# Optimization experiments

Hardware: AMD Instinct MI355X
Metric: run time of the kernel (lower is better)

Reference implementation:

```python
import jax, jax.numpy as jnp
import numpy as np

DIM = 512
NUM_HEADS = 8
HEAD_DIM = DIM // NUM_HEADS
SCALE = HEAD_DIM ** -0.5


def setup_inputs() -> dict:
    key = jax.random.key(0)
    k_x, k_qkv, k_proj, k_pb = jax.random.split(key, 4)
    x = jax.random.normal(k_x, (2, 4096, DIM), dtype=jnp.float32)
    # nn.Linear weights: stored as [out, in]; qkv_bias=False so no qkv bias.
    w_qkv = jax.random.normal(k_qkv, (3 * DIM, DIM), dtype=jnp.float32) * (DIM ** -0.5)
    w_proj = jax.random.normal(k_proj, (DIM, DIM), dtype=jnp.float32) * (DIM ** -0.5)
    b_proj = jax.random.normal(k_pb, (DIM,), dtype=jnp.float32) * 0.01
    return {"x": x, "w_qkv": w_qkv, "w_proj": w_proj, "b_proj": b_proj}


def reference(x, w_qkv, w_proj, b_proj):
    B, N, D = x.shape
    H, Hd = NUM_HEADS, HEAD_DIM
    # qkv: [B, N, 3D] -> [3, B, H, N, Hd]
    qkv = (x @ w_qkv.T).reshape(B, N, 3, H, Hd).transpose(2, 0, 3, 1, 4)
    q, k, v = qkv[0], qkv[1], qkv[2]
    # Naive full attention matrix in fp32 (matches original non-fused path).
    attn = jnp.einsum('bhqd,bhkd->bhqk', q, k) * SCALE
    attn = jax.nn.softmax(attn, axis=-1)
    out = jnp.einsum('bhqk,bhkd->bhqd', attn, v)
    out = out.transpose(0, 2, 1, 3).reshape(B, N, D)
    return out @ w_proj.T + b_proj
```

## Files before the change

### kernel.cpp

```cpp
#include <hip/hip_runtime.h>
#include <stdint.h>

#define SEQ   4096
#define DIMM  512
#define HDIM  64
#define NH    8
#define ROWS  8192
#define QKVN  1536

typedef __attribute__((ext_vector_type(8))) __bf16 bf16x8;
typedef __attribute__((ext_vector_type(4))) float  f32x4;
typedef __attribute__((ext_vector_type(4))) uint32_t u32x4;

__device__ __forceinline__ uint32_t cvtpk(float lo, float hi) {
  uint32_t w;
  asm("v_cvt_pk_bf16_f32 %0, %1, %2" : "=v"(w) : "v"(lo), "v"(hi));
  return w;
}

__device__ __forceinline__ void swap32(uint32_t& a, uint32_t& b) {
  asm("v_permlane32_swap_b32 %0, %1" : "+v"(a), "+v"(b));
}
__device__ __forceinline__ void swap16(uint32_t& a, uint32_t& b) {
  asm("v_permlane16_swap_b32 %0, %1" : "+v"(a), "+v"(b));
}

__device__ __forceinline__ f32x4 mfma16(bf16x8 a, bf16x8 b, f32x4 c) {
  return __builtin_amdgcn_mfma_f32_16x16x32_bf16(a, b, c, 0, 0, 0);
}

#if __has_builtin(__builtin_amdgcn_exp2f)
#define EXP2F(x) __builtin_amdgcn_exp2f(x)
#else
#define EXP2F(x) exp2f(x)
#endif

__device__ __forceinline__ void gld16(const void* g, void* l) {
  __builtin_amdgcn_global_load_lds(
      (const __attribute__((address_space(1))) uint32_t*)g,
      (__attribute__((address_space(3))) uint32_t*)l, 16, 0, 0);
}

#define X4  (ROWS * DIMM / 4)
#define Q4  (QKVN * DIMM / 4)
#define P4  (DIMM * DIMM / 4)

__global__ __launch_bounds__(256) void cvt_kernel(
    const float* __restrict__ x, const float* __restrict__ wq,
    const float* __restrict__ wp, uint16_t* __restrict__ xb,
    uint16_t* __restrict__ wqb, uint16_t* __restrict__ wpb) {
  int idx = blockIdx.x * 256 + threadIdx.x;
  const float* src; uint16_t* dst; int i4;
  if (idx < X4)            { src = x;  dst = xb;  i4 = idx; }
  else if (idx < X4 + Q4)  { src = wq; dst = wqb; i4 = idx - X4; }
  else                     { src = wp; dst = wpb; i4 = idx - X4 - Q4; }
  float4 v = ((const float4*)src)[i4];
  uint2 o;
  o.x = cvtpk(v.x, v.y);
  o.y = cvtpk(v.z, v.w);
  ((uint2*)dst)[i4] = o;
}

__device__ __forceinline__ void gemm_core(
    int bm, int bn,
    const uint16_t* __restrict__ A, const uint16_t* __restrict__ B,
    uint16_t (*As)[128 * 32], uint16_t (*Bs)[128 * 32], f32x4 acc[4][4]) {
  const int tid = threadIdx.x;
  const int lane = tid & 63, wave = tid >> 6;
  const int quad = lane >> 4, l16 = lane & 15;
  const int wr = (wave & 1) * 64, wc = (wave >> 1) * 64;
  const int sw = (l16 >> 1) & 3;

  auto stage = [&](int buf, int kt) {
#pragma unroll
    for (int it = 0; it < 2; ++it) {
      int L = it * 256 + tid;
      int r = L >> 2, c = L & 3;
      int gc = c ^ ((r >> 1) & 3);
      int ldsoff = (it * 256 + (tid & ~63)) * 16;
      gld16((const char*)A + ((size_t)(bm * 128 + r) * DIMM + kt * 32) * 2 + gc * 16,
            (char*)As[buf] + ldsoff);
      gld16((const char*)B + ((size_t)(bn * 128 + r) * DIMM + kt * 32) * 2 + gc * 16,
            (char*)Bs[buf] + ldsoff);
    }
  };

  stage(0, 0);
  for (int kt = 0; kt < DIMM / 32; ++kt) {
    const int cur = kt & 1;
    __syncthreads();
    if (kt < DIMM / 32 - 1) stage(cur ^ 1, kt + 1);

    bf16x8 af[4], bfr[4];
#pragma unroll
    for (int i = 0; i < 4; ++i)
      af[i] = *(const bf16x8*)(As[cur] + (wr + i * 16 + l16) * 32 + ((quad ^ sw) * 8));
#pragma unroll
    for (int j = 0; j < 4; ++j)
      bfr[j] = *(const bf16x8*)(Bs[cur] + (wc + j * 16 + l16) * 32 + ((quad ^ sw) * 8));
    __builtin_amdgcn_s_setprio(1);
#pragma unroll
    for (int i = 0; i < 4; ++i)
#pragma unroll
      for (int j = 0; j < 4; ++j)
        acc[i][j] = mfma16(af[i], bfr[j], acc[i][j]);
    __builtin_amdgcn_s_setprio(0);
  }
}

__global__ __launch_bounds__(256, 4) void qkv_gemm(
    const uint16_t* __restrict__ xb, const uint16_t* __restrict__ wqb,
    uint16_t* __restrict__ qd, uint16_t* __restrict__ kd,
    uint16_t* __restrict__ vt) {
  __shared__ __align__(16) uint16_t As[2][128 * 32];
  __shared__ __align__(16) uint16_t Bs[2][128 * 32];
  const int lin = blockIdx.y * 64 + blockIdx.x;
  const int bm = (lin & 7) * 8 + ((lin >> 3) / 12);
  const int bn = (lin >> 3) % 12;
  f32x4 acc[4][4];
#pragma unroll
  for (int i = 0; i < 4; ++i)
#pragma unroll
    for (int j = 0; j < 4; ++j) acc[i][j] = f32x4{0.f, 0.f, 0.f, 0.f};

  gemm_core(bm, bn, xb, wqb, As, Bs, acc);

  const int lane = threadIdx.x & 63, wave = threadIdx.x >> 6;
  const int quad = lane >> 4, l16 = lane & 15;
  const int wr = (wave & 1) * 64, wc = (wave >> 1) * 64;
  const float qscale = 0.125f * 1.44269504f;
#pragma unroll
  for (int i = 0; i < 4; ++i) {
    int m0 = bm * 128 + wr + i * 16 + quad * 4;
    int b = m0 >> 12, n0 = m0 & 4095;
#pragma unroll
    for (int j = 0; j < 4; ++j) {
      int jc = bn * 128 + wc + j * 16 + l16;
      int region = jc >> 9;
      int h = (jc >> 6) & 7, hd = jc & 63;
      int bh = (b << 3) | h;
      if (region == 0) {
        uint32_t w01 = cvtpk(acc[i][j][0] * qscale, acc[i][j][1] * qscale);
        uint32_t w23 = cvtpk(acc[i][j][2] * qscale, acc[i][j][3] * qscale);
        size_t rb = ((size_t)bh * SEQ + n0) * HDIM + hd;
        qd[rb]            = (uint16_t)w01;
        qd[rb + HDIM]     = (uint16_t)(w01 >> 16);
        qd[rb + 2 * HDIM] = (uint16_t)w23;
        qd[rb + 3 * HDIM] = (uint16_t)(w23 >> 16);
      } else if (region == 1) {
        uint32_t w01 = cvtpk(acc[i][j][0], acc[i][j][1]);
        uint32_t w23 = cvtpk(acc[i][j][2], acc[i][j][3]);
        size_t rb = ((size_t)bh * SEQ + n0) * HDIM + hd;
        kd[rb]            = (uint16_t)w01;
        kd[rb + HDIM]     = (uint16_t)(w01 >> 16);
        kd[rb + 2 * HDIM] = (uint16_t)w23;
        kd[rb + 3 * HDIM] = (uint16_t)(w23 >> 16);
      } else {
        uint2 pk;
        pk.x = cvtpk(acc[i][j][0], acc[i][j][1]);
        pk.y = cvtpk(acc[i][j][2], acc[i][j][3]);
        *(uint2*)(vt + ((size_t)bh * HDIM + hd) * SEQ + n0) = pk;
      }
    }
  }
}

__global__ __launch_bounds__(512, 4) void attn_kernel(
    const uint16_t* __restrict__ qd, const uint16_t* __restrict__ kd,
    const uint16_t* __restrict__ vt, uint16_t* __restrict__ ao) {
  __shared__ __align__(16) uint16_t Ks[2][128 * 64];
  __shared__ __align__(16) uint16_t Vs[2][64 * 128];

  const int tid = threadIdx.x, lane = tid & 63, wave = tid >> 6;
  const int quad = lane >> 4, l16 = lane & 15;
  const int pair = wave >> 1, khalf = wave & 1;
  const int wid = blockIdx.x;
  const int xcd = wid & 7, slot = wid >> 3;
  const int bh = xcd + 8 * (slot & 1);
  const int qt = slot >> 1;
  const size_t base_qk = (size_t)bh * SEQ * HDIM;
  const size_t base_v  = (size_t)bh * HDIM * SEQ;
  const int sw7 = l16 & 7;

  auto stage = [&](int buf, int kt) {
#pragma unroll
    for (int it = 0; it < 2; ++it) {
      int L = it * 512 + tid;
      int ldsoff = (it * 512 + (tid & ~63)) * 16;
      int rk = L >> 3, ck = L & 7;
      int gck = ck ^ (rk & 7);
      gld16((const char*)kd + (base_qk + (size_t)(kt * 128 + rk) * HDIM) * 2 + gck * 16,
            (char*)Ks[buf] + ldsoff);
      int rv = L >> 4, cv = L & 15;
      int gcv = cv ^ (rv & 15);
      gld16((const char*)vt + (base_v + (size_t)rv * SEQ + (size_t)kt * 128) * 2 + gcv * 16,
            (char*)Vs[buf] + ldsoff);
    }
  };

  bf16x8 qf[2][2];
#pragma unroll
  for (int it2 = 0; it2 < 2; ++it2)
#pragma unroll
    for (int kh = 0; kh < 2; ++kh)
      qf[it2][kh] = *(const bf16x8*)(qd + base_qk +
          (size_t)(qt * 128 + pair * 32 + it2 * 16 + l16) * HDIM + kh * 32 + quad * 8);

  const u32x4 onesw = {0x3F803F80u, 0x3F803F80u, 0x3F803F80u, 0x3F803F80u};
  const bf16x8 onesf = __builtin_bit_cast(bf16x8, onesw);

  f32x4 O[2][4];
  f32x4 Lacc[2];
#pragma unroll
  for (int a = 0; a < 2; ++a) {
    Lacc[a] = f32x4{0.f, 0.f, 0.f, 0.f};
#pragma unroll
    for (int d = 0; d < 4; ++d) O[a][d] = f32x4{0.f, 0.f, 0.f, 0.f};
  }

  stage(0, 0);
  for (int kt = 0; kt < SEQ / 128; ++kt) {
    const int cur = kt & 1;
    __syncthreads();
    if (kt < SEQ / 128 - 1) stage(cur ^ 1, kt + 1);

    bf16x8 kf[4][2];
#pragma unroll
    for (int jh = 0; jh < 4; ++jh) {
      int jf = khalf * 4 + jh;
      const uint16_t* krow = Ks[cur] + (jf * 16 + l16) * 64;
      kf[jh][0] = *(const bf16x8*)(krow + ((quad ^ sw7) * 8));
      kf[jh][1] = *(const bf16x8*)(krow + (((4 + quad) ^ sw7) * 8));
    }

    f32x4 P[4][2];
    __builtin_amdgcn_s_setprio(1);
#pragma unroll
    for (int jh = 0; jh < 4; ++jh)
#pragma unroll
      for (int it2 = 0; it2 < 2; ++it2) {
        f32x4 s = f32x4{0.f, 0.f, 0.f, 0.f};
        s = mfma16(kf[jh][0], qf[it2][0], s);
        s = mfma16(kf[jh][1], qf[it2][1], s);
        P[jh][it2] = s;
      }
    __builtin_amdgcn_s_setprio(0);

    uint32_t sp[4][2][2];
#pragma unroll
    for (int jh = 0; jh < 4; ++jh)
#pragma unroll
      for (int it2 = 0; it2 < 2; ++it2) {
        float p0 = EXP2F(P[jh][it2][0]);
        float p1 = EXP2F(P[jh][it2][1]);
        float p2 = EXP2F(P[jh][it2][2]);
        float p3 = EXP2F(P[jh][it2][3]);
        sp[jh][it2][0] = cvtpk(p0, p1);
        sp[jh][it2][1] = cvtpk(p2, p3);
      }

    bf16x8 pb[2][2];
#pragma unroll
    for (int kp = 0; kp < 2; ++kp)
#pragma unroll
      for (int it2 = 0; it2 < 2; ++it2) {
        uint32_t t0 = sp[2 * kp][it2][0], t2 = sp[2 * kp + 1][it2][0];
        swap32(t0, t2); swap16(t0, t2);
        uint32_t t1 = sp[2 * kp][it2][1], t3 = sp[2 * kp + 1][it2][1];
        swap32(t1, t3); swap16(t1, t3);
        u32x4 w = {t0, t1, t2, t3};
        pb[kp][it2] = __builtin_bit_cast(bf16x8, w);
      }

#pragma unroll
    for (int kp = 0; kp < 2; ++kp) {
      bf16x8 va[4];
#pragma unroll
      for (int dl = 0; dl < 4; ++dl)
        va[dl] = *(const bf16x8*)((const char*)Vs[cur] + (dl * 16 + l16) * 256 +
                                  (((khalf * 8 + kp * 4 + quad) ^ l16) & 15) * 16);
      __builtin_amdgcn_s_setprio(1);
#pragma unroll
      for (int it2 = 0; it2 < 2; ++it2) {
        Lacc[it2] = mfma16(onesf, pb[kp][it2], Lacc[it2]);
#pragma unroll
        for (int dl = 0; dl < 4; ++dl)
          O[it2][dl] = mfma16(va[dl], pb[kp][it2], O[it2][dl]);
      }
      __builtin_amdgcn_s_setprio(0);
    }
  }

  float lsum[2] = {Lacc[0][0], Lacc[1][0]};

  __syncthreads();
  if (!(wave & 1)) {
    f32x4* ob = (f32x4*)((char*)Ks + pair * 8192);
#pragma unroll
    for (int it2 = 0; it2 < 2; ++it2)
#pragma unroll
      for (int dl = 0; dl < 4; ++dl)
        ob[(it2 * 4 + dl) * 64 + lane] = O[it2][dl];
    float2* lb = (float2*)((char*)Vs + pair * 512);
    lb[lane] = make_float2(lsum[0], lsum[1]);
  }
  __syncthreads();
  if (wave & 1) {
    const f32x4* ob = (const f32x4*)((char*)Ks + pair * 8192);
    float2 lp = ((const float2*)((char*)Vs + pair * 512))[lane];
    lsum[0] += lp.x; lsum[1] += lp.y;
#pragma unroll
    for (int it2 = 0; it2 < 2; ++it2)
#pragma unroll
      for (int dl = 0; dl < 4; ++dl)
        O[it2][dl] += ob[(it2 * 4 + dl) * 64 + lane];

    const int b = bh >> 3, h = bh & 7;
#pragma unroll
    for (int it2 = 0; it2 < 2; ++it2) {
      float inv = 1.0f / lsum[it2];
      int q = qt * 128 + pair * 32 + it2 * 16 + l16;
      size_t rowbase = ((size_t)(b * SEQ + q)) * DIMM + h * HDIM;
#pragma unroll
      for (int dl = 0; dl < 4; ++dl) {
        uint2 pk;
        pk.x = cvtpk(O[it2][dl][0] * inv, O[it2][dl][1] * inv);
        pk.y = cvtpk(O[it2][dl][2] * inv, O[it2][dl][3] * inv);
        *(uint2*)(ao + rowbase + dl * 16 + quad * 4) = pk;
      }
    }
  }
}

__global__ __launch_bounds__(256, 4) void proj_gemm(
    const uint16_t* __restrict__ ao, const uint16_t* __restrict__ wpb,
    const float* __restrict__ bprj, float* __restrict__ out) {
  __shared__ __align__(16) uint16_t As[2][64 * 32];
  __shared__ __align__(16) uint16_t Bs[2][128 * 32];
  const int lin = blockIdx.y * 128 + blockIdx.x;
  const int idx = lin >> 3;
  const int bm = (lin & 7) * 16 + (idx >> 2);
  const int bn = idx & 3;

  const int tid = threadIdx.x;
  const int lane = tid & 63, wave = tid >> 6;
  const int quad = lane >> 4, l16 = lane & 15;
  const int wc = wave * 32;
  const int sw = (l16 >> 1) & 3;

  f32x4 acc[4][2];
#pragma unroll
  for (int i = 0; i < 4; ++i)
#pragma unroll
    for (int j = 0; j < 2; ++j) acc[i][j] = f32x4{0.f, 0.f, 0.f, 0.f};

  auto stage = [&](int buf, int kt) {
    {
      int r = tid >> 2, c = tid & 3;
      int gc = c ^ ((r >> 1) & 3);
      int ldsoff = (tid & ~63) * 16;
      gld16((const char*)ao + ((size_t)(bm * 64 + r) * DIMM + kt * 32) * 2 + gc * 16,
            (char*)As[buf] + ldsoff);
    }
#pragma unroll
    for (int it = 0; it < 2; ++it) {
      int L = it * 256 + tid;
      int r = L >> 2, c = L & 3;
      int gc = c ^ ((r >> 1) & 3);
      int ldsoff = (it * 256 + (tid & ~63)) * 16;
      gld16((const char*)wpb + ((size_t)(bn * 128 + r) * DIMM + kt * 32) * 2 + gc * 16,
            (char*)Bs[buf] + ldsoff);
    }
  };

  stage(0, 0);
  for (int kt = 0; kt < DIMM / 32; ++kt) {
    const int cur = kt & 1;
    __syncthreads();
    if (kt < DIMM / 32 - 1) stage(cur ^ 1, kt + 1);

    bf16x8 af[4], bfr[2];
#pragma unroll
    for (int i = 0; i < 4; ++i)
      af[i] = *(const bf16x8*)(As[cur] + (i * 16 + l16) * 32 + ((quad ^ sw) * 8));
#pragma unroll
    for (int j = 0; j < 2; ++j)
      bfr[j] = *(const bf16x8*)(Bs[cur] + (wc + j * 16 + l16) * 32 + ((quad ^ sw) * 8));
    __builtin_amdgcn_s_setprio(1);
#pragma unroll
    for (int i = 0; i < 4; ++i)
#pragma unroll
      for (int j = 0; j < 2; ++j)
        acc[i][j] = mfma16(af[i], bfr[j], acc[i][j]);
    __builtin_amdgcn_s_setprio(0);
  }

#pragma unroll
  for (int i = 0; i < 4; ++i) {
    int m0 = bm * 64 + i * 16 + quad * 4;
#pragma unroll
    for (int j = 0; j < 2; ++j) {
      int jc = bn * 128 + wc + j * 16 + l16;
      float bias = bprj[jc];
#pragma unroll
      for (int r = 0; r < 4; ++r)
        out[(size_t)(m0 + r) * DIMM + jc] = acc[i][j][r] + bias;
    }
  }
}

extern "C" void kernel_launch(void* const* d_in, const int* in_sizes, int n_in,
                              void* d_out, int out_size, void* d_ws, size_t ws_size,
                              hipStream_t stream) {
  const float* x     = (const float*)d_in[0];
  const float* wqkv  = (const float*)d_in[1];
  const float* wproj = (const float*)d_in[2];
  const float* bproj = (const float*)d_in[3];

  char* ws = (char*)d_ws;
  uint16_t* xb  = (uint16_t*)(ws + 0);
  uint16_t* wqb = (uint16_t*)(ws + 8388608);
  uint16_t* wpb = (uint16_t*)(ws + 9961472);
  uint16_t* qd  = (uint16_t*)(ws + 10485760);
  uint16_t* kd  = (uint16_t*)(ws + 18874368);
  uint16_t* vt  = (uint16_t*)(ws + 27262976);
  uint16_t* ao  = (uint16_t*)(ws + 35651584);

  cvt_kernel<<<(X4 + Q4 + P4) / 256, 256, 0, stream>>>(x, wqkv, wproj, xb, wqb, wpb);
  qkv_gemm<<<dim3(64, 12), 256, 0, stream>>>(xb, wqb, qd, kd, vt);
  attn_kernel<<<512, 512, 0, stream>>>(qd, kd, vt, ao);
  proj_gemm<<<dim3(128, 4), 256, 0, stream>>>(ao, wpb, bproj, (float*)d_out);
}
```

Measured before the change: 179.5 us.

## Fuse fp32-to-bf16 conversion of x into the QKV GEMM A-tile loads

Removes the separate conversion of the activation x from the conversion kernel. The QKV GEMM now reads fp32 x directly into registers, converts it to bf16 and writes it to LDS, with the next tile's loads overlapping the current MFMAs. This drops a full write and re-read of the bf16 copy of x (16MB fp32 read plus 8MB write plus 8MB read becomes only the fp32 read repeated per N-tile). In exchange, each of the 12 column blocks re-reads x in fp32 (twice the bytes), registers rise, and occupancy hint drops from 4 to 3.

```diff
diff --git a/kernel.cpp b/kernel.cpp
--- a/kernel.cpp
+++ b/kernel.cpp
@@ -41,19 +41,16 @@
       (__attribute__((address_space(3))) uint32_t*)l, 16, 0, 0);
 }
 
-#define X4  (ROWS * DIMM / 4)
 #define Q4  (QKVN * DIMM / 4)
 #define P4  (DIMM * DIMM / 4)
 
 __global__ __launch_bounds__(256) void cvt_kernel(
-    const float* __restrict__ x, const float* __restrict__ wq,
-    const float* __restrict__ wp, uint16_t* __restrict__ xb,
+    const float* __restrict__ wq, const float* __restrict__ wp,
     uint16_t* __restrict__ wqb, uint16_t* __restrict__ wpb) {
   int idx = blockIdx.x * 256 + threadIdx.x;
   const float* src; uint16_t* dst; int i4;
-  if (idx < X4)            { src = x;  dst = xb;  i4 = idx; }
-  else if (idx < X4 + Q4)  { src = wq; dst = wqb; i4 = idx - X4; }
-  else                     { src = wp; dst = wpb; i4 = idx - X4 - Q4; }
+  if (idx < Q4) { src = wq; dst = wqb; i4 = idx; }
+  else          { src = wp; dst = wpb; i4 = idx - Q4; }
   float4 v = ((const float4*)src)[i4];
   uint2 o;
   o.x = cvtpk(v.x, v.y);
@@ -61,55 +58,8 @@
   ((uint2*)dst)[i4] = o;
 }
 
-__device__ __forceinline__ void gemm_core(
-    int bm, int bn,
-    const uint16_t* __restrict__ A, const uint16_t* __restrict__ B,
-    uint16_t (*As)[128 * 32], uint16_t (*Bs)[128 * 32], f32x4 acc[4][4]) {
-  const int tid = threadIdx.x;
-  const int lane = tid & 63, wave = tid >> 6;
-  const int quad = lane >> 4, l16 = lane & 15;
-  const int wr = (wave & 1) * 64, wc = (wave >> 1) * 64;
-  const int sw = (l16 >> 1) & 3;
-
-  auto stage = [&](int buf, int kt) {
-#pragma unroll
-    for (int it = 0; it < 2; ++it) {
-      int L = it * 256 + tid;
-      int r = L >> 2, c = L & 3;
-      int gc = c ^ ((r >> 1) & 3);
-      int ldsoff = (it * 256 + (tid & ~63)) * 16;
-      gld16((const char*)A + ((size_t)(bm * 128 + r) * DIMM + kt * 32) * 2 + gc * 16,
-            (char*)As[buf] + ldsoff);
-      gld16((const char*)B + ((size_t)(bn * 128 + r) * DIMM + kt * 32) * 2 + gc * 16,
-            (char*)Bs[buf] + ldsoff);
-    }
-  };
-
-  stage(0, 0);
-  for (int kt = 0; kt < DIMM / 32; ++kt) {
-    const int cur = kt & 1;
-    __syncthreads();
-    if (kt < DIMM / 32 - 1) stage(cur ^ 1, kt + 1);
-
-    bf16x8 af[4], bfr[4];
-#pragma unroll
-    for (int i = 0; i < 4; ++i)
-      af[i] = *(const bf16x8*)(As[cur] + (wr + i * 16 + l16) * 32 + ((quad ^ sw) * 8));
-#pragma unroll
-    for (int j = 0; j < 4; ++j)
-      bfr[j] = *(const bf16x8*)(Bs[cur] + (wc + j * 16 + l16) * 32 + ((quad ^ sw) * 8));
-    __builtin_amdgcn_s_setprio(1);
-#pragma unroll
-    for (int i = 0; i < 4; ++i)
-#pragma unroll
-      for (int j = 0; j < 4; ++j)
-        acc[i][j] = mfma16(af[i], bfr[j], acc[i][j]);
-    __builtin_amdgcn_s_setprio(0);
-  }
-}
-
-__global__ __launch_bounds__(256, 4) void qkv_gemm(
-    const uint16_t* __restrict__ xb, const uint16_t* __restrict__ wqb,
+__global__ __launch_bounds__(256, 3) void qkv_gemm(
+    const float* __restrict__ x, const uint16_t* __restrict__ wqb,
     uint16_t* __restrict__ qd, uint16_t* __restrict__ kd,
     uint16_t* __restrict__ vt) {
   __shared__ __align__(16) uint16_t As[2][128 * 32];
@@ -117,17 +67,78 @@
   const int lin = blockIdx.y * 64 + blockIdx.x;
   const int bm = (lin & 7) * 8 + ((lin >> 3) / 12);
   const int bn = (lin >> 3) % 12;
-  f32x4 acc[4][4];
-#pragma unroll
-  for (int i = 0; i < 4; ++i)
-#pragma unroll
-    for (int j = 0; j < 4; ++j) acc[i][j] = f32x4{0.f, 0.f, 0.f, 0.f};
-
-  gemm_core(bm, bn, xb, wqb, As, Bs, acc);
-
-  const int lane = threadIdx.x & 63, wave = threadIdx.x >> 6;
+
+  const int tid = threadIdx.x;
+  const int lane = tid & 63, wave = tid >> 6;
   const int quad = lane >> 4, l16 = lane & 15;
   const int wr = (wave & 1) * 64, wc = (wave >> 1) * 64;
+  const int sw = (l16 >> 1) & 3;
+
+  f32x4 acc[4][4];
+#pragma unroll
+  for (int i = 0; i < 4; ++i)
+#pragma unroll
+    for (int j = 0; j < 4; ++j) acc[i][j] = f32x4{0.f, 0.f, 0.f, 0.f};
+
+  auto stageB = [&](int buf, int kt) {
+#pragma unroll
+    for (int it = 0; it < 2; ++it) {
+      int L = it * 256 + tid;
+      int r = L >> 2, c = L & 3;
+      int gc = c ^ ((r >> 1) & 3);
+      int ldsoff = (it * 256 + (tid & ~63)) * 16;
+      gld16((const char*)wqb + ((size_t)(bn * 128 + r) * DIMM + kt * 32) * 2 + gc * 16,
+            (char*)Bs[buf] + ldsoff);
+    }
+  };
+  auto loadA = [&](int kt, float4 (&av)[4]) {
+#pragma unroll
+    for (int it = 0; it < 2; ++it) {
+      int L = it * 256 + tid;
+      int r = L >> 2, c = L & 3;
+      int gc = c ^ ((r >> 1) & 3);
+      const float* src = x + (size_t)(bm * 128 + r) * DIMM + kt * 32 + gc * 8;
+      av[it * 2]     = *(const float4*)(src);
+      av[it * 2 + 1] = *(const float4*)(src + 4);
+    }
+  };
+  auto writeA = [&](int buf, float4 (&av)[4]) {
+#pragma unroll
+    for (int it = 0; it < 2; ++it) {
+      int L = it * 256 + tid;
+      u32x4 w;
+      w.x = cvtpk(av[it * 2].x,     av[it * 2].y);
+      w.y = cvtpk(av[it * 2].z,     av[it * 2].w);
+      w.z = cvtpk(av[it * 2 + 1].x, av[it * 2 + 1].y);
+      w.w = cvtpk(av[it * 2 + 1].z, av[it * 2 + 1].w);
+      *(u32x4*)((char*)As[buf] + L * 16) = w;
+    }
+  };
+
+  float4 av[4];
+  loadA(0, av); writeA(0, av); stageB(0, 0);
+  for (int kt = 0; kt < DIMM / 32; ++kt) {
+    const int cur = kt & 1;
+    __syncthreads();
+    if (kt < DIMM / 32 - 1) { loadA(kt + 1, av); stageB(cur ^ 1, kt + 1); }
+
+    bf16x8 af[4], bfr[4];
+#pragma unroll
+    for (int i = 0; i < 4; ++i)
+      af[i] = *(const bf16x8*)(As[cur] + (wr + i * 16 + l16) * 32 + ((quad ^ sw) * 8));
+#pragma unroll
+    for (int j = 0; j < 4; ++j)
+      bfr[j] = *(const bf16x8*)(Bs[cur] + (wc + j * 16 + l16) * 32 + ((quad ^ sw) * 8));
+    __builtin_amdgcn_s_setprio(1);
+#pragma unroll
+    for (int i = 0; i < 4; ++i)
+#pragma unroll
+      for (int j = 0; j < 4; ++j)
+        acc[i][j] = mfma16(af[i], bfr[j], acc[i][j]);
+    __builtin_amdgcn_s_setprio(0);
+    if (kt < DIMM / 32 - 1) writeA(cur ^ 1, av);
+  }
+
   const float qscale = 0.125f * 1.44269504f;
 #pragma unroll
   for (int i = 0; i < 4; ++i) {
@@ -418,7 +429,6 @@
   const float* bproj = (const float*)d_in[3];
 
   char* ws = (char*)d_ws;
-  uint16_t* xb  = (uint16_t*)(ws + 0);
   uint16_t* wqb = (uint16_t*)(ws + 8388608);
   uint16_t* wpb = (uint16_t*)(ws + 9961472);
   uint16_t* qd  = (uint16_t*)(ws + 10485760);
@@ -426,8 +436,8 @@
   uint16_t* vt  = (uint16_t*)(ws + 27262976);
   uint16_t* ao  = (uint16_t*)(ws + 35651584);
 
-  cvt_kernel<<<(X4 + Q4 + P4) / 256, 256, 0, stream>>>(x, wqkv, wproj, xb, wqb, wpb);
-  qkv_gemm<<<dim3(64, 12), 256, 0, stream>>>(xb, wqb, qd, kd, vt);
+  cvt_kernel<<<(Q4 + P4) / 256, 256, 0, stream>>>(wqkv, wproj, wqb, wpb);
+  qkv_gemm<<<dim3(64, 12), 256, 0, stream>>>(x, wqb, qd, kd, vt);
   attn_kernel<<<512, 512, 0, stream>>>(qd, kd, vt, ao);
   proj_gemm<<<dim3(128, 4), 256, 0, stream>>>(ao, wpb, bproj, (float*)d_out);
 }
```

Result: no change. 177.7 us (median of 2 runs) (-1.0%).
